# Kernel optimization log

Measured on AMD Instinct MI355X. Metric: run time of the kernel, lower is better.

## Reference

```python
import jax, jax.numpy as jnp
import numpy as np

N, E, H, D, C, L = 20000, 320000, 8, 64, 512, 2  # nodes, edges, heads, head_dim, channels, layers


def layer_norm(x, g, b, eps=1e-5):
    mu = x.mean(-1, keepdims=True)
    var = ((x - mu) ** 2).mean(-1, keepdims=True)
    return (x - mu) / jnp.sqrt(var + eps) * g + b


def setup_inputs() -> dict:
    key = jax.random.key(0)
    ks = jax.random.split(key, 14)
    s = 0.02
    x = jax.random.normal(ks[0], (N, C), jnp.float32)
    edge_index = jax.random.randint(ks[1], (2, E), 0, N, jnp.int32)
    edge_type = jax.random.randint(ks[2], (E,), 0, 10, jnp.int32)
    edge_repre = jax.random.normal(ks[3], (E,), jnp.float32)
    # Per-layer TransformerConv params (query/key/value/skip linears, each with bias)
    Wq = jax.random.normal(ks[4], (L, C, C), jnp.float32) * s
    Wk = jax.random.normal(ks[5], (L, C, C), jnp.float32) * s
    Wv = jax.random.normal(ks[6], (L, C, C), jnp.float32) * s
    Ws = jax.random.normal(ks[7], (L, C, C), jnp.float32) * s
    bq = jnp.zeros((L, C), jnp.float32)
    bk = jnp.zeros((L, C), jnp.float32)
    bv = jnp.zeros((L, C), jnp.float32)
    bs = jnp.zeros((L, C), jnp.float32)
    # FFN + shared LayerNorm
    W1 = jax.random.normal(ks[8], (C, 2 * C), jnp.float32) * s
    b1 = jnp.zeros((2 * C,), jnp.float32)
    W2 = jax.random.normal(ks[9], (2 * C, C), jnp.float32) * s
    b2 = jnp.zeros((C,), jnp.float32)
    ln_g = jnp.ones((C,), jnp.float32)
    ln_b = jnp.zeros((C,), jnp.float32)
    return {"x": x, "edge_index": edge_index, "edge_type": edge_type, "edge_repre": edge_repre,
            "Wq": Wq, "bq": bq, "Wk": Wk, "bk": bk, "Wv": Wv, "bv": bv, "Ws": Ws, "bs": bs,
            "W1": W1, "b1": b1, "W2": W2, "b2": b2, "ln_g": ln_g, "ln_b": ln_b}


def reference(x, edge_index, edge_type, edge_repre, Wq, bq, Wk, bk, Wv, bv, Ws, bs, W1, b1, W2, b2, ln_g, ln_b):
    src, dst = edge_index[0], edge_index[1]  # messages flow src -> dst (PyG source_to_target)
    enc = x
    scale = 1.0 / jnp.sqrt(jnp.float32(D))
    for l in range(L):
        q = (x @ Wq[l] + bq[l]).reshape(N, H, D)
        k = (x @ Wk[l] + bk[l]).reshape(N, H, D)
        v = (x @ Wv[l] + bv[l]).reshape(N, H, D)
        # per-edge attention logits [E, H]
        a = (q[dst] * k[src]).sum(-1) * scale
        # segment softmax over edges sharing a destination node
        amax = jax.ops.segment_max(a, dst, num_segments=N)
        amax = jnp.where(jnp.isfinite(amax), amax, 0.0)
        e = jnp.exp(a - amax[dst])
        denom = jax.ops.segment_sum(e, dst, num_segments=N)
        alpha = e / (denom[dst] + 1e-16)
        # scatter-aggregate weighted values, concat heads
        agg = jax.ops.segment_sum(alpha[:, :, None] * v[src], dst, num_segments=N).reshape(N, C)
        # root/skip connection (beta=False) + module-level residual to enc_emb
        x = agg + (x @ Ws[l] + bs[l]) + enc
    x = layer_norm(x, ln_g, ln_b)
    x = (jax.nn.relu(x @ W1 + b1) @ W2 + b2) + x
    x = layer_norm(x, ln_g, ln_b)
    return x + enc
```

## Files before the change

kernel.cpp:

```cpp
#include <hip/hip_runtime.h>

typedef __attribute__((ext_vector_type(8))) short short8;
typedef __attribute__((ext_vector_type(4))) float f32x4;

__device__ __forceinline__ unsigned short f2b(float f){
  union { float f; unsigned u; } x; x.f = f;
  unsigned r = x.u + 0x7fffu + ((x.u >> 16) & 1u);
  return (unsigned short)(r >> 16);
}
__device__ __forceinline__ float b2f(unsigned short v){
  union { unsigned u; float f; } x; x.u = ((unsigned)v) << 16; return x.f;
}

__device__ __forceinline__ int pslot(int t){
  return (t & ~7) | ((t & 3) << 1) | ((t >> 2) & 1);
}

__device__ __forceinline__ unsigned char enc1(float v){
#if __has_builtin(__builtin_amdgcn_cvt_pk_fp8_f32)
  return (unsigned char)(__builtin_amdgcn_cvt_pk_fp8_f32(v, v, 0, false) & 0xff);
#else
  union{float f;unsigned u;}x; x.f=v;
  unsigned s = x.u >> 31;
  float av = fabsf(v);
  if (av >= 448.f) return (unsigned char)((s<<7)|0x7e);
  if (av < 0.0078125f){ unsigned d=(unsigned)(av*512.f+0.5f); return (unsigned char)((s<<7)|d); }
  unsigned q = x.u & 0x7fffffff;
  q = q + 0x7ffff + ((q>>20)&1);
  int e2 = (int)(q>>23) - 127;
  unsigned m3 = (q>>20)&7;
  if (e2 < -6){ unsigned d=(unsigned)(av*512.f+0.5f); return (unsigned char)((s<<7)|d); }
  return (unsigned char)((s<<7) | ((unsigned)(e2+7)<<3) | m3);
#endif
}
__device__ __forceinline__ unsigned pk4(float a,float b,float c,float d){
#if __has_builtin(__builtin_amdgcn_cvt_pk_fp8_f32)
  int v = __builtin_amdgcn_cvt_pk_fp8_f32(a, b, 0, false);
  v = __builtin_amdgcn_cvt_pk_fp8_f32(c, d, v, true);
  return (unsigned)v;
#else
  return (unsigned)enc1(a) | ((unsigned)enc1(b)<<8) | ((unsigned)enc1(c)<<16) | ((unsigned)enc1(d)<<24);
#endif
}
__device__ __forceinline__ void dec4(unsigned u, float* o){
#if __has_builtin(__builtin_amdgcn_cvt_pk_f32_fp8)
  auto lo = __builtin_amdgcn_cvt_pk_f32_fp8((int)u, false);
  auto hi = __builtin_amdgcn_cvt_pk_f32_fp8((int)u, true);
  o[0]=lo[0]; o[1]=lo[1]; o[2]=hi[0]; o[3]=hi[1];
#else
  #pragma unroll
  for (int j=0;j<4;j++){
    unsigned b = (u >> (8*j)) & 0xffu;
    unsigned s = b >> 7, ex = (b >> 3) & 15u, mn = b & 7u;
    union{unsigned u;float f;} x;
    x.u = ex ? ((s<<31)|((ex+120u)<<23)|(mn<<20)) : (s<<31);
    o[j] = x.f;
  }
#endif
}

__global__ void count_k(const int* __restrict__ dst, int* __restrict__ deg, int E){
  int e = blockIdx.x*256 + threadIdx.x;
  if (e < E) atomicAdd(&deg[dst[e]], 1);
}

__global__ void scan_k(const int* __restrict__ deg, int* __restrict__ rowstart,
                       int* __restrict__ cursor, int n)
{
  __shared__ int wsum[16];
  int tid = threadIdx.x, lane = tid & 63, wv = tid >> 6;
  int CH = (n + 1023) >> 10;
  int b0 = tid * CH; if (b0 > n) b0 = n;
  int bend = b0 + CH; if (bend > n) bend = n;
  int sum = 0;
  for (int i = b0; i < bend; ++i) sum += deg[i];
  int xs = sum;
  #pragma unroll
  for (int o=1;o<64;o<<=1){ int t = __shfl_up(xs, o, 64); if (lane >= o) xs += t; }
  if (lane == 63) wsum[wv] = xs;
  __syncthreads();
  if (tid < 16){
    int w = wsum[tid];
    #pragma unroll
    for (int o=1;o<16;o<<=1){ int t = __shfl_up(w, o, 64); if (tid >= o) w += t; }
    wsum[tid] = w;
  }
  __syncthreads();
  int off = (wv ? wsum[wv-1] : 0) + xs - sum;
  int run = off;
  for (int i = b0; i < bend; ++i){ rowstart[i] = run; cursor[i] = run; run += deg[i]; }
  if (b0 < n && bend == n) rowstart[n] = run;
  if (n == 0 && tid == 0) rowstart[0] = 0;
}

__global__ void fill_k(const int* __restrict__ src, const int* __restrict__ dst,
                       int* __restrict__ cursor, int* __restrict__ csrc, int E){
  int e = blockIdx.x*256 + threadIdx.x;
  if (e < E){
    int p = atomicAdd(&cursor[dst[e]], 1);
    csrc[p] = src[e];
  }
}

__global__ void transpose_all_k(const float* __restrict__ Wq, const float* __restrict__ Wk,
  const float* __restrict__ Wv, const float* __restrict__ Ws,
  const float* __restrict__ W1, const float* __restrict__ W2,
  unsigned char* __restrict__ wtqkvs8, unsigned char* __restrict__ wt1_8,
  unsigned char* __restrict__ wt2_8)
{
  int bid = blockIdx.x;
  const float* src; unsigned char* dst; int r, c, lb;
  if (bid < 1024){
    int j = bid >> 7;
    int l = j >> 2, w = j & 3;
    src = (w==0?Wq : w==1?Wk : w==2?Wv : Ws) + (size_t)l*512*512;
    dst = wtqkvs8 + ((size_t)l*2048 + (size_t)w*512)*512;
    r = 512; c = 512; lb = bid & 127;
  } else if (bid < 1280){ src = W1; dst = wt1_8; r = 512; c = 1024; lb = bid - 1024; }
  else { src = W2; dst = wt2_8; r = 1024; c = 512; lb = bid - 1280; }
  int idx = lb*256 + threadIdx.x;
  int o = idx % c;
  int i0 = (idx / c) << 3;
  float v[8];
  #pragma unroll
  for (int t=0;t<8;t++) v[t] = 64.f * src[(size_t)(i0+t)*c + o];
  unsigned lo = pk4(v[0],v[1],v[2],v[3]);
  unsigned hi = pk4(v[4],v[5],v[6],v[7]);
  *(unsigned long long*)&dst[(size_t)o*r + pslot(i0>>3)*8] =
      (unsigned long long)lo | ((unsigned long long)hi << 32);
}

__global__ void cvt8_k(const float* __restrict__ in, unsigned char* __restrict__ out8,
                       unsigned short* __restrict__ outb, size_t n){
  size_t i = ((size_t)blockIdx.x*256 + threadIdx.x)*8;
  if (i >= n) return;
  const float4* p = (const float4*)(in + i);
  float4 a0 = p[0], a1 = p[1];
  short8 vv;
  ((unsigned short*)&vv)[0] = f2b(a0.x); ((unsigned short*)&vv)[1] = f2b(a0.y);
  ((unsigned short*)&vv)[2] = f2b(a0.z); ((unsigned short*)&vv)[3] = f2b(a0.w);
  ((unsigned short*)&vv)[4] = f2b(a1.x); ((unsigned short*)&vv)[5] = f2b(a1.y);
  ((unsigned short*)&vv)[6] = f2b(a1.z); ((unsigned short*)&vv)[7] = f2b(a1.w);
  *(short8*)&outb[i] = vv;
  unsigned lo = pk4(a0.x,a0.y,a0.z,a0.w);
  unsigned hi = pk4(a1.x,a1.y,a1.z,a1.w);
  size_t op = (i & ~(size_t)511) | ((size_t)pslot((int)((i & 511) >> 3)) << 3);
  *(unsigned long long*)&out8[op] = (unsigned long long)lo | ((unsigned long long)hi<<32);
}

template<int MODE, int KC, int NN>
__global__ __launch_bounds__(256) void gemm8_k(
    const unsigned char* __restrict__ A8,
    const unsigned char* __restrict__ Bt8,
    int M,
    const float* __restrict__ bias0, const float* __restrict__ bias1,
    const float* __restrict__ bias2, const float* __restrict__ bias3,
    unsigned short* __restrict__ qb, unsigned short* __restrict__ skipb,
    unsigned char* __restrict__ outC,
    float* __restrict__ outF, const float* __restrict__ res)
{
  __shared__ __align__(16) unsigned char lA[128*128];
  __shared__ __align__(16) unsigned char lB[128*128];
  const int tid  = threadIdx.x;
  const int lane = tid & 63;
  const int wid  = tid >> 6;

  const int nwg = gridDim.x;
  int id = blockIdx.x;
  int q = nwg >> 3, r = nwg & 7;
  int xc = id & 7, yy = id >> 3;
  int swz = (xc < r ? xc*(q+1) : r*(q+1) + (xc-r)*q) + yy;
  const int bm = (swz / NN) * 128;
  const int bn = (swz % NN) * 128;
  const int wm = (wid >> 1) * 64;
  const int wn = (wid & 1) * 64;

  f32x4 acc[4][4];
  #pragma unroll
  for (int m=0;m<4;m++)
    #pragma unroll
    for (int n=0;n<4;n++) acc[m][n] = (f32x4)0.f;

  const int kq = lane >> 4;

  for (int kt = 0; kt < KC; kt += 128){
    #pragma unroll
    for (int it = 0; it < 4; ++it) {
      int chunk = it*256 + tid;
      int row = chunk >> 3;
      int cin = chunk & 7;
      int scol = (cin ^ (row & 7)) * 16;
      int ga = bm + row; if (ga >= M) ga = M - 1;
      __builtin_amdgcn_global_load_lds(
        (const __attribute__((address_space(1))) void*)(A8 + (size_t)ga*KC + kt + scol),
        (__attribute__((address_space(3))) void*)(&lA[(it*256 + (wid<<6))*16]),
        16, 0, 0);
      __builtin_amdgcn_global_load_lds(
        (const __attribute__((address_space(1))) void*)(Bt8 + (size_t)(bn + row)*KC + kt + scol),
        (__attribute__((address_space(3))) void*)(&lB[(it*256 + (wid<<6))*16]),
        16, 0, 0);
    }
    __syncthreads();
    #pragma unroll
    for (int S = 0; S < 2; ++S){
      ulonglong2 af[4], bfv[4];
      #pragma unroll
      for (int m=0;m<4;m++){
        int rr = wm + m*16 + (lane & 15);
        int c  = (S*4 + kq) ^ (rr & 7);
        af[m] = *(const ulonglong2*)&lA[rr*128 + c*16];
      }
      #pragma unroll
      for (int n=0;n<4;n++){
        int rr = wn + n*16 + (lane & 15);
        int c  = (S*4 + kq) ^ (rr & 7);
        bfv[n] = *(const ulonglong2*)&lB[rr*128 + c*16];
      }
      #pragma unroll
      for (int m=0;m<4;m++)
        #pragma unroll
        for (int n=0;n<4;n++){
          acc[m][n] = __builtin_amdgcn_mfma_f32_16x16x32_fp8_fp8(
              (long)af[m].x, (long)bfv[n].x, acc[m][n], 0,0,0);
          acc[m][n] = __builtin_amdgcn_mfma_f32_16x16x32_fp8_fp8(
              (long)af[m].y, (long)bfv[n].y, acc[m][n], 0,0,0);
        }
    }
    __syncthreads();
  }

  #pragma unroll
  for (int m=0;m<4;m++){
    int row0 = bm + wm + m*16 + ((lane >> 4) << 2);
    #pragma unroll
    for (int n=0;n<4;n++){
      int col = bn + wn + n*16 + (lane & 15);
      float bval;
      if (MODE == 0){
        bval = (col < 512) ? bias0[col]
             : (col < 1024) ? bias1[col-512]
             : (col < 1536) ? bias2[col-1024] : bias3[col-1536];
      } else {
        bval = bias0[col];
      }
      #pragma unroll
      for (int r4=0;r4<4;r4++){
        int row = row0 + r4;
        if (row < M){
          float v = acc[m][n][r4] * 0.015625f + bval;
          if (MODE == 0){
            if (col < 512)       qb[(size_t)row*512 + col] = f2b(v);
            else if (col < 1536) outC[(size_t)row*1024 + (col-512)] = enc1(v);
            else                 skipb[(size_t)row*512 + (col-1536)] = f2b(v);
          } else if (MODE == 1){
            v = fmaxf(v, 0.0f);
            int pc = (col & ~7) | 0;
            pc = (pslot(col >> 3) << 3) | (col & 7);
            outC[(size_t)row*1024 + pc] = enc1(v);
          } else {
            v += res[(size_t)row*512 + col];
            outF[(size_t)row*512 + col] = v;
          }
        }
      }
    }
  }
}

template<int OUT>
__global__ __launch_bounds__(256) void attn_k(
  const unsigned short* __restrict__ qb, const unsigned char* __restrict__ kv8,
  const unsigned short* __restrict__ skipb, const unsigned short* __restrict__ encb,
  const int* __restrict__ rowstart, const int* __restrict__ csrc,
  float* __restrict__ xout, unsigned char* __restrict__ xout8, int N)
{
  int n = blockIdx.x*4 + (threadIdx.x>>6);
  if (n >= N) return;
  int lane = threadIdx.x & 63;
  const short8 qv = *(const short8*)&qb[(size_t)n*512 + lane*8];
  float qf[8];
  #pragma unroll
  for (int j=0;j<8;j++) qf[j] = b2f(((const unsigned short*)&qv)[j]);
  float m = -__builtin_inff(), l = 0.f;
  float acc[8] = {0.f,0.f,0.f,0.f,0.f,0.f,0.f,0.f};
  int e = rowstart[n], e1 = rowstart[n+1];
  if (e < e1){
    int s = csrc[e];
    uint2 kc = *(const uint2*)&kv8[(size_t)s*1024 + lane*8];
    uint2 vc = *(const uint2*)&kv8[(size_t)s*1024 + 512 + lane*8];
    for (; e < e1; ++e){
      int sn = (e+1 < e1) ? csrc[e+1] : s;
      uint2 kn = *(const uint2*)&kv8[(size_t)sn*1024 + lane*8];
      uint2 vn = *(const uint2*)&kv8[(size_t)sn*1024 + 512 + lane*8];
      float kf[8]; dec4(kc.x, kf); dec4(kc.y, kf+4);
      float dot = 0.f;
      #pragma unroll
      for (int j=0;j<8;j++) dot += qf[j]*kf[j];
      dot += __shfl_xor(dot,1); dot += __shfl_xor(dot,2); dot += __shfl_xor(dot,4);
      float a = dot * 0.125f;
      float mn2 = fmaxf(m, a);
      float corr = __expf(m - mn2);
      float p = __expf(a - mn2);
      l = l*corr + p;
      float vf[8]; dec4(vc.x, vf); dec4(vc.y, vf+4);
      #pragma unroll
      for (int j=0;j<8;j++) acc[j] = acc[j]*corr + p*vf[j];
      m = mn2;
      kc = kn; vc = vn;
    }
  }
  float inv = 1.f/(l + 1e-16f);
  size_t base = (size_t)n*512 + (size_t)lane*8;
  const short8 sv = *(const short8*)&skipb[base];
  const short8 ev = *(const short8*)&encb[base];
  float o[8];
  #pragma unroll
  for (int j=0;j<8;j++)
    o[j] = acc[j]*inv + b2f(((const unsigned short*)&sv)[j]) + b2f(((const unsigned short*)&ev)[j]);
  if (OUT == 0){
    unsigned lo = pk4(o[0],o[1],o[2],o[3]);
    unsigned hi = pk4(o[4],o[5],o[6],o[7]);
    size_t op = (size_t)n*512 + ((size_t)pslot(lane) << 3);
    *(unsigned long long*)&xout8[op] = (unsigned long long)lo | ((unsigned long long)hi<<32);
  } else {
    float4* po = (float4*)&xout[base];
    po[0] = make_float4(o[0],o[1],o[2],o[3]);
    po[1] = make_float4(o[4],o[5],o[6],o[7]);
  }
}

template<int MODE>
__global__ __launch_bounds__(256) void ln_k(const float* __restrict__ x,
  const float* __restrict__ g, const float* __restrict__ b,
  float* __restrict__ outF, unsigned char* __restrict__ out8,
  const float* __restrict__ addv, int N)
{
  int n = blockIdx.x*4 + (threadIdx.x>>6);
  if (n >= N) return;
  int lane = threadIdx.x & 63;
  size_t base = (size_t)n*512 + (size_t)lane*8;
  const float4* p = (const float4*)(x + base);
  float4 a0 = p[0], a1 = p[1];
  float v[8] = {a0.x,a0.y,a0.z,a0.w,a1.x,a1.y,a1.z,a1.w};
  float s=0.f, ss=0.f;
  #pragma unroll
  for (int j=0;j<8;j++){ s += v[j]; ss += v[j]*v[j]; }
  #pragma unroll
  for (int o=1;o<64;o<<=1){ s += __shfl_xor(s,o); ss += __shfl_xor(ss,o); }
  float mean = s * (1.f/512.f);
  float var  = ss * (1.f/512.f) - mean*mean;
  float rstd = rsqrtf(var + 1e-5f);
  float o[8];
  #pragma unroll
  for (int j=0;j<8;j++){
    int c = lane*8 + j;
    o[j] = (v[j]-mean)*rstd*g[c] + b[c];
  }
  if (MODE == 0){
    float4* po = (float4*)&outF[base];
    po[0] = make_float4(o[0],o[1],o[2],o[3]);
    po[1] = make_float4(o[4],o[5],o[6],o[7]);
    unsigned lo = pk4(o[0],o[1],o[2],o[3]);
    unsigned hi = pk4(o[4],o[5],o[6],o[7]);
    size_t op = (size_t)n*512 + ((size_t)pslot(lane) << 3);
    *(unsigned long long*)&out8[op] = (unsigned long long)lo | ((unsigned long long)hi<<32);
  } else {
    #pragma unroll
    for (int j=0;j<8;j++) outF[base+j] = o[j] + addv[base+j];
  }
}

extern "C" void kernel_launch(void* const* d_in, const int* in_sizes, int n_in,
                              void* d_out, int out_size, void* d_ws, size_t ws_size,
                              hipStream_t stream)
{
  const float* x0  = (const float*)d_in[0];
  const int*  eidx = (const int*)d_in[1];
  const float* Wq  = (const float*)d_in[4];
  const float* bq  = (const float*)d_in[5];
  const float* Wk  = (const float*)d_in[6];
  const float* bk  = (const float*)d_in[7];
  const float* Wv  = (const float*)d_in[8];
  const float* bv  = (const float*)d_in[9];
  const float* Wsk = (const float*)d_in[10];
  const float* bs  = (const float*)d_in[11];
  const float* W1  = (const float*)d_in[12];
  const float* b1  = (const float*)d_in[13];
  const float* W2  = (const float*)d_in[14];
  const float* b2  = (const float*)d_in[15];
  const float* lng = (const float*)d_in[16];
  const float* lnb = (const float*)d_in[17];

  const int N = in_sizes[0] / 512;
  const int E = in_sizes[1] / 2;
  const int* esrc = eidx;
  const int* edst = eidx + E;

  char* ws = (char*)d_ws;
  size_t off = 0;
  auto alloc = [&](size_t bytes)->char*{
    char* p = ws + off; off = (off + bytes + 255) & ~(size_t)255; return p;
  };
  unsigned char*  wtqkvs8 = (unsigned char*)alloc((size_t)2*2048*512);
  unsigned char*  wt1_8   = (unsigned char*)alloc((size_t)1024*512);
  unsigned char*  wt2_8   = (unsigned char*)alloc((size_t)512*1024);
  unsigned short* qb      = (unsigned short*)alloc((size_t)N*512*2);
  unsigned char*  kv8     = (unsigned char*)alloc((size_t)N*1024);
  float*          skip    = (float*)alloc((size_t)N*512*4);
  float*          xbuf    = (float*)alloc((size_t)N*512*4);
  unsigned char*  xb8     = (unsigned char*)alloc((size_t)N*512);
  unsigned short* encb    = (unsigned short*)alloc((size_t)N*512*2);
  unsigned short* skipb   = (unsigned short*)alloc((size_t)N*512*2);
  int* deg      = (int*)alloc((size_t)N*4);
  int* rowstart = (int*)alloc((size_t)(N+1)*4);
  int* cursor   = (int*)alloc((size_t)N*4);
  int* csrc     = (int*)alloc((size_t)E*4);
  unsigned char* t8 = (unsigned char*)qb;
  unsigned char* h8 = xb8;

  hipMemsetAsync(deg, 0, (size_t)N*4, stream);
  count_k<<<(E+255)/256, 256, 0, stream>>>(edst, deg, E);
  scan_k<<<1, 1024, 0, stream>>>(deg, rowstart, cursor, N);
  fill_k<<<(E+255)/256, 256, 0, stream>>>(esrc, edst, cursor, csrc, E);

  transpose_all_k<<<1536, 256, 0, stream>>>(Wq, Wk, Wv, Wsk, W1, W2, wtqkvs8, wt1_8, wt2_8);

  const int cvtBlocks = (int)(((size_t)N*512/8 + 255)/256);
  const int rowBlocks = (N + 3)/4;
  const int MB = (N + 127)/128;

  cvt8_k<<<cvtBlocks, 256, 0, stream>>>(x0, xb8, encb, (size_t)N*512);
  for (int l = 0; l < 2; ++l){
    gemm8_k<0,512,16><<<MB*16, 256, 0, stream>>>(xb8, wtqkvs8 + (size_t)l*2048*512, N,
        bq + l*512, bk + l*512, bv + l*512, bs + l*512, qb, skipb, kv8, nullptr, nullptr);
    if (l == 0)
      attn_k<0><<<rowBlocks, 256, 0, stream>>>(qb, kv8, skipb, encb, rowstart, csrc, nullptr, xb8, N);
    else
      attn_k<1><<<rowBlocks, 256, 0, stream>>>(qb, kv8, skipb, encb, rowstart, csrc, xbuf, nullptr, N);
  }

  ln_k<0><<<rowBlocks, 256, 0, stream>>>(xbuf, lng, lnb, skip, h8, nullptr, N);
  gemm8_k<1,512,8><<<MB*8, 256, 0, stream>>>(h8, wt1_8, N,
      b1, nullptr, nullptr, nullptr, nullptr, nullptr, t8, nullptr, nullptr);
  gemm8_k<2,1024,4><<<MB*4, 256, 0, stream>>>(t8, wt2_8, N,
      b2, nullptr, nullptr, nullptr, nullptr, nullptr, nullptr, xbuf, skip);
  ln_k<1><<<rowBlocks, 256, 0, stream>>>(xbuf, lng, lnb, (float*)d_out, nullptr, x0, N);
}
```

Baseline: 458.7 us.

## Make attention kernel persistent with atomic node queue, deeper prefetch, no max tracking

Result: slower. 932.4 us (+103.3%).

```diff
diff --git a/kernel.cpp b/kernel.cpp
--- a/kernel.cpp
+++ b/kernel.cpp
@@ -254,8 +254,7 @@
             else                 skipb[(size_t)row*512 + (col-1536)] = f2b(v);
           } else if (MODE == 1){
             v = fmaxf(v, 0.0f);
-            int pc = (col & ~7) | 0;
-            pc = (pslot(col >> 3) << 3) | (col & 7);
+            int pc = (pslot(col >> 3) << 3) | (col & 7);
             outC[(size_t)row*1024 + pc] = enc1(v);
           } else {
             v += res[(size_t)row*512 + col];
@@ -272,60 +271,66 @@
   const unsigned short* __restrict__ qb, const unsigned char* __restrict__ kv8,
   const unsigned short* __restrict__ skipb, const unsigned short* __restrict__ encb,
   const int* __restrict__ rowstart, const int* __restrict__ csrc,
-  float* __restrict__ xout, unsigned char* __restrict__ xout8, int N)
-{
-  int n = blockIdx.x*4 + (threadIdx.x>>6);
-  if (n >= N) return;
+  float* __restrict__ xout, unsigned char* __restrict__ xout8,
+  int* __restrict__ cursor, int N)
+{
   int lane = threadIdx.x & 63;
-  const short8 qv = *(const short8*)&qb[(size_t)n*512 + lane*8];
-  float qf[8];
-  #pragma unroll
-  for (int j=0;j<8;j++) qf[j] = b2f(((const unsigned short*)&qv)[j]);
-  float m = -__builtin_inff(), l = 0.f;
-  float acc[8] = {0.f,0.f,0.f,0.f,0.f,0.f,0.f,0.f};
-  int e = rowstart[n], e1 = rowstart[n+1];
-  if (e < e1){
-    int s = csrc[e];
-    uint2 kc = *(const uint2*)&kv8[(size_t)s*1024 + lane*8];
-    uint2 vc = *(const uint2*)&kv8[(size_t)s*1024 + 512 + lane*8];
-    for (; e < e1; ++e){
-      int sn = (e+1 < e1) ? csrc[e+1] : s;
-      uint2 kn = *(const uint2*)&kv8[(size_t)sn*1024 + lane*8];
-      uint2 vn = *(const uint2*)&kv8[(size_t)sn*1024 + 512 + lane*8];
-      float kf[8]; dec4(kc.x, kf); dec4(kc.y, kf+4);
-      float dot = 0.f;
-      #pragma unroll
-      for (int j=0;j<8;j++) dot += qf[j]*kf[j];
-      dot += __shfl_xor(dot,1); dot += __shfl_xor(dot,2); dot += __shfl_xor(dot,4);
-      float a = dot * 0.125f;
-      float mn2 = fmaxf(m, a);
-      float corr = __expf(m - mn2);
-      float p = __expf(a - mn2);
-      l = l*corr + p;
-      float vf[8]; dec4(vc.x, vf); dec4(vc.y, vf+4);
-      #pragma unroll
-      for (int j=0;j<8;j++) acc[j] = acc[j]*corr + p*vf[j];
-      m = mn2;
-      kc = kn; vc = vn;
+  for (;;){
+    int n;
+    if (lane == 0) n = atomicAdd(cursor, 1);
+    n = __shfl(n, 0, 64);
+    if (n >= N) return;
+
+    const short8 qv = *(const short8*)&qb[(size_t)n*512 + lane*8];
+    size_t base = (size_t)n*512 + (size_t)lane*8;
+    const short8 sv = *(const short8*)&skipb[base];
+    const short8 ev = *(const short8*)&encb[base];
+    float qf[8];
+    #pragma unroll
+    for (int j=0;j<8;j++) qf[j] = b2f(((const unsigned short*)&qv)[j]);
+
+    float l = 0.f;
+    float acc[8] = {0.f,0.f,0.f,0.f,0.f,0.f,0.f,0.f};
+    int e = rowstart[n], e1 = rowstart[n+1];
+    if (e < e1){
+      int s0 = csrc[e];
+      int s1 = (e+1 < e1) ? csrc[e+1] : s0;
+      uint2 k0 = *(const uint2*)&kv8[(size_t)s0*1024 + lane*8];
+      uint2 v0 = *(const uint2*)&kv8[(size_t)s0*1024 + 512 + lane*8];
+      uint2 k1 = *(const uint2*)&kv8[(size_t)s1*1024 + lane*8];
+      uint2 v1 = *(const uint2*)&kv8[(size_t)s1*1024 + 512 + lane*8];
+      for (; e < e1; ++e){
+        int s2 = (e+2 < e1) ? csrc[e+2] : s0;
+        uint2 k2 = *(const uint2*)&kv8[(size_t)s2*1024 + lane*8];
+        uint2 v2 = *(const uint2*)&kv8[(size_t)s2*1024 + 512 + lane*8];
+        float kf[8]; dec4(k0.x, kf); dec4(k0.y, kf+4);
+        float dot = 0.f;
+        #pragma unroll
+        for (int j=0;j<8;j++) dot += qf[j]*kf[j];
+        dot += __shfl_xor(dot,1); dot += __shfl_xor(dot,2); dot += __shfl_xor(dot,4);
+        float p = __expf(dot * 0.125f);
+        l += p;
+        float vf[8]; dec4(v0.x, vf); dec4(v0.y, vf+4);
+        #pragma unroll
+        for (int j=0;j<8;j++) acc[j] += p*vf[j];
+        k0 = k1; v0 = v1; k1 = k2; v1 = v2;
+      }
     }
-  }
-  float inv = 1.f/(l + 1e-16f);
-  size_t base = (size_t)n*512 + (size_t)lane*8;
-  const short8 sv = *(const short8*)&skipb[base];
-  const short8 ev = *(const short8*)&encb[base];
-  float o[8];
-  #pragma unroll
-  for (int j=0;j<8;j++)
-    o[j] = acc[j]*inv + b2f(((const unsigned short*)&sv)[j]) + b2f(((const unsigned short*)&ev)[j]);
-  if (OUT == 0){
-    unsigned lo = pk4(o[0],o[1],o[2],o[3]);
-    unsigned hi = pk4(o[4],o[5],o[6],o[7]);
-    size_t op = (size_t)n*512 + ((size_t)pslot(lane) << 3);
-    *(unsigned long long*)&xout8[op] = (unsigned long long)lo | ((unsigned long long)hi<<32);
-  } else {
-    float4* po = (float4*)&xout[base];
-    po[0] = make_float4(o[0],o[1],o[2],o[3]);
-    po[1] = make_float4(o[4],o[5],o[6],o[7]);
+    float inv = 1.f/(l + 1e-16f);
+    float o[8];
+    #pragma unroll
+    for (int j=0;j<8;j++)
+      o[j] = acc[j]*inv + b2f(((const unsigned short*)&sv)[j]) + b2f(((const unsigned short*)&ev)[j]);
+    if (OUT == 0){
+      unsigned lo = pk4(o[0],o[1],o[2],o[3]);
+      unsigned hi = pk4(o[4],o[5],o[6],o[7]);
+      size_t op = (size_t)n*512 + ((size_t)pslot(lane) << 3);
+      *(unsigned long long*)&xout8[op] = (unsigned long long)lo | ((unsigned long long)hi<<32);
+    } else {
+      float4* po = (float4*)&xout[base];
+      po[0] = make_float4(o[0],o[1],o[2],o[3]);
+      po[1] = make_float4(o[4],o[5],o[6],o[7]);
+    }
   }
 }
 
@@ -415,10 +420,12 @@
   int* rowstart = (int*)alloc((size_t)(N+1)*4);
   int* cursor   = (int*)alloc((size_t)N*4);
   int* csrc     = (int*)alloc((size_t)E*4);
+  int* acur     = (int*)alloc(256);
   unsigned char* t8 = (unsigned char*)qb;
   unsigned char* h8 = xb8;
 
   hipMemsetAsync(deg, 0, (size_t)N*4, stream);
+  hipMemsetAsync(acur, 0, 8, stream);
   count_k<<<(E+255)/256, 256, 0, stream>>>(edst, deg, E);
   scan_k<<<1, 1024, 0, stream>>>(deg, rowstart, cursor, N);
   fill_k<<<(E+255)/256, 256, 0, stream>>>(esrc, edst, cursor, csrc, E);
@@ -434,9 +441,11 @@
     gemm8_k<0,512,16><<<MB*16, 256, 0, stream>>>(xb8, wtqkvs8 + (size_t)l*2048*512, N,
         bq + l*512, bk + l*512, bv + l*512, bs + l*512, qb, skipb, kv8, nullptr, nullptr);
     if (l == 0)
-      attn_k<0><<<rowBlocks, 256, 0, stream>>>(qb, kv8, skipb, encb, rowstart, csrc, nullptr, xb8, N);
+      attn_k<0><<<1024, 256, 0, stream>>>(qb, kv8, skipb, encb, rowstart, csrc,
+          nullptr, xb8, acur, N);
     else
-      attn_k<1><<<rowBlocks, 256, 0, stream>>>(qb, kv8, skipb, encb, rowstart, csrc, xbuf, nullptr, N);
+      attn_k<1><<<1024, 256, 0, stream>>>(qb, kv8, skipb, encb, rowstart, csrc,
+          xbuf, nullptr, acur + 1, N);
   }
 
   ln_k<0><<<rowBlocks, 256, 0, stream>>>(xbuf, lng, lnb, skip, h8, nullptr, N);
```
